# Optimization experiments

Hardware: AMD Instinct MI355X
Metric: run time of the kernel (lower is better)

The kernel has to match this reference:

```python
import jax, jax.numpy as jnp
import numpy as np

N = 50000      # num nodes
E = 800000     # num edges (avg degree 16)
IN_FEA = 256
OU_FEA = 64


def setup_inputs() -> dict:
    key = jax.random.key(0)
    k_h, k_w, k_r, k_c, k_v = jax.random.split(key, 5)
    h = jax.random.normal(k_h, (N, IN_FEA), dtype=jnp.float32)
    # Linear(in_fea, ou_fea, bias=None): weight applied as h @ W, W [IN, OUT]
    W = jax.random.normal(k_w, (IN_FEA, OU_FEA), dtype=jnp.float32) / np.sqrt(IN_FEA)
    row = jax.random.randint(k_r, (E,), 0, N, dtype=jnp.int32)
    col = jax.random.randint(k_c, (E,), 0, N, dtype=jnp.int32)
    vals = jax.random.uniform(k_v, (E,), dtype=jnp.float32)
    return {"h": h, "W": W, "row": row, "col": col, "vals": vals}


def reference(h, W, row, col, vals):
    # dense projection: [N, IN] @ [IN, OUT] -> [N, OUT]
    hp = h @ W
    # torch builds sparse tensor with indices [col, row], i.e. G = A^T,
    # so torch.sparse.mm(G, hp)[i] = sum over edges with col==i of vals * hp[row]
    msg = hp[row] * vals[:, None]                      # [E, OUT] gather + scale
    out = jax.ops.segment_sum(msg, col, num_segments=N)  # scatter-add to dest
    return out
```

## Files before the change

kernel.cpp:

```cpp
#include <hip/hip_runtime.h>
#include <hip/hip_bf16.h>

#define IN_F 256
#define OU_F 64
#define BKN 128
#define BSHIFT 7
#define NBMAX 512
#define CHUNK 4096
#define STAGE_CAP 4096

typedef __attribute__((ext_vector_type(8))) short short8;
typedef __attribute__((ext_vector_type(4))) float f32x4;

__device__ inline short8 cvt8(float4 a, float4 b)
{
    union { short8 s8; __hip_bfloat162 h2[4]; } u;
    u.h2[0] = __float22bfloat162_rn(make_float2(a.x, a.y));
    u.h2[1] = __float22bfloat162_rn(make_float2(a.z, a.w));
    u.h2[2] = __float22bfloat162_rn(make_float2(b.x, b.y));
    u.h2[3] = __float22bfloat162_rn(make_float2(b.z, b.w));
    return u.s8;
}

__global__ void __launch_bounds__(512, 4)
gemm_mfma_kernel(const float* __restrict__ h, const float* __restrict__ W,
                 __hip_bfloat16* __restrict__ hp, int* __restrict__ bcnt,
                 int N, int ntiles)
{
    __shared__ unsigned short Wt[64][264];
    const int t = threadIdx.x;

    if (blockIdx.x == 0)
        for (int i = t; i <= NBMAX; i += 512) bcnt[i] = 0;

#pragma unroll
    for (int i = 0; i < 16; ++i) {
        int p  = t + i * 512;
        int c  = p & 63;
        int k0 = (p >> 6) << 1;
        float x = W[(size_t)k0 * OU_F + c];
        float y = W[(size_t)(k0 + 1) * OU_F + c];
        __hip_bfloat162 bb = __float22bfloat162_rn(make_float2(x, y));
        *reinterpret_cast<unsigned*>(&Wt[c][k0]) = *reinterpret_cast<unsigned*>(&bb);
    }
    __syncthreads();

    const int l   = t & 63;
    const int wv  = t >> 6;
    const int cl  = l & 15;
    const int kg  = l >> 4;
    const int rg4 = wv & 3;
    const int cg  = wv >> 2;

    short8 bfr[2][8];
#pragma unroll
    for (int nt2 = 0; nt2 < 2; ++nt2)
#pragma unroll
        for (int ks = 0; ks < 8; ++ks)
            bfr[nt2][ks] = *reinterpret_cast<const short8*>(
                &Wt[cg * 32 + nt2 * 16 + cl][ks * 32 + kg * 8]);

    for (int tile = blockIdx.x; tile < ntiles; tile += gridDim.x) {
        const int rbase = tile * 64 + rg4 * 16;
        const int r     = rbase + cl;
        const int rld   = min(r, N - 1);
        const float4* hrow = reinterpret_cast<const float4*>(h) + (size_t)rld * (IN_F / 4);

        f32x4 acc0 = (f32x4){0.f, 0.f, 0.f, 0.f};
        f32x4 acc1 = (f32x4){0.f, 0.f, 0.f, 0.f};
#pragma unroll
        for (int ks = 0; ks < 8; ++ks) {
            float4 a0 = hrow[ks * 8 + kg * 2];
            float4 a1 = hrow[ks * 8 + kg * 2 + 1];
            short8 af = cvt8(a0, a1);
            acc0 = __builtin_amdgcn_mfma_f32_16x16x32_bf16(af, bfr[0][ks], acc0, 0, 0, 0);
            acc1 = __builtin_amdgcn_mfma_f32_16x16x32_bf16(af, bfr[1][ks], acc1, 0, 0, 0);
        }

#pragma unroll
        for (int rg = 0; rg < 4; ++rg) {
            int rr = rbase + kg * 4 + rg;
            if (rr < N) {
                size_t base = (size_t)rr * OU_F + cg * 32 + cl;
                hp[base]      = __float2bfloat16(acc0[rg]);
                hp[base + 16] = __float2bfloat16(acc1[rg]);
            }
        }
    }
}

__global__ void __launch_bounds__(256)
hist_scan_kernel(const int* __restrict__ col, int* __restrict__ bcnt,
                 int* __restrict__ boffs, int* __restrict__ bcursor, int E, int NB)
{
    __shared__ int lh[NBMAX];
    __shared__ int s[256];
    __shared__ int isLast;
    const int t = threadIdx.x;

    for (int i = t; i < NB; i += 256) lh[i] = 0;
    __syncthreads();

    const int n4 = E >> 2;
    const int4* c4 = (const int4*)col;
    for (int i = blockIdx.x * 256 + t; i < n4; i += gridDim.x * 256) {
        int4 v = c4[i];
        atomicAdd(&lh[v.x >> BSHIFT], 1);
        atomicAdd(&lh[v.y >> BSHIFT], 1);
        atomicAdd(&lh[v.z >> BSHIFT], 1);
        atomicAdd(&lh[v.w >> BSHIFT], 1);
    }
    if (blockIdx.x == 0)
        for (int e = (n4 << 2) + t; e < E; e += 256)
            atomicAdd(&lh[col[e] >> BSHIFT], 1);
    __syncthreads();

    for (int i = t; i < NB; i += 256)
        if (lh[i]) atomicAdd(&bcnt[i], lh[i]);

    __threadfence();
    if (t == 0) {
        int v = atomicAdd(&bcnt[NBMAX], 1);
        isLast = (v == (int)gridDim.x - 1);
    }
    __syncthreads();
    if (!isLast) return;

    for (int i = t; i < NB; i += 256)
        lh[i] = __hip_atomic_load(&bcnt[i], __ATOMIC_RELAXED, __HIP_MEMORY_SCOPE_AGENT);
    __syncthreads();

    int idx = t * 2;
    int c0 = (idx     < NB) ? lh[idx]     : 0;
    int c1 = (idx + 1 < NB) ? lh[idx + 1] : 0;
    int s0 = c0, s1 = s0 + c1;
    s[t] = s1;
    __syncthreads();
    for (int d = 1; d < 256; d <<= 1) {
        int v = (t >= d) ? s[t - d] : 0;
        __syncthreads();
        s[t] += v;
        __syncthreads();
    }
    int excl = (t > 0) ? s[t - 1] : 0;
    if (idx     < NB) { boffs[idx]     = excl;      bcursor[idx]     = excl;      }
    if (idx + 1 < NB) { boffs[idx + 1] = excl + s0; bcursor[idx + 1] = excl + s0; }
    if (t == 255) boffs[NB] = s[255];
}

__global__ void __launch_bounds__(256)
partition_kernel(const int* __restrict__ row, const int* __restrict__ col,
                 const float* __restrict__ vals, int* __restrict__ bcursor,
                 int2* __restrict__ epk, int E, int NB)
{
    __shared__ int  hist[NBMAX];
    __shared__ int  X[NBMAX];
    __shared__ int  gshift[NBMAX];
    __shared__ int  s[256];
    __shared__ int2 stage[CHUNK];
    __shared__ int  gpos[CHUNK];

    const int t = threadIdx.x;
    const int base = blockIdx.x * CHUNK;
    const int n = min(CHUNK, E - base);

    for (int i = t; i < NBMAX; i += 256) hist[i] = 0;
    __syncthreads();

#pragma unroll
    for (int k = 0; k < CHUNK / 256; ++k) {
        int i = t + k * 256;
        if (i < n) atomicAdd(&hist[col[base + i] >> BSHIFT], 1);
    }
    __syncthreads();

    int idx = t * 2;
    int c0 = hist[idx], c1 = hist[idx + 1];
    int s0 = c0, s1 = s0 + c1;
    s[t] = s1;
    __syncthreads();
    for (int d = 1; d < 256; d <<= 1) {
        int v = (t >= d) ? s[t - d] : 0;
        __syncthreads();
        s[t] += v;
        __syncthreads();
    }
    int excl = (t > 0) ? s[t - 1] : 0;
    X[idx]     = excl;
    X[idx + 1] = excl + s0;
    __syncthreads();

    for (int i = t; i < NB; i += 256) {
        int hcnt = hist[i];
        int g = hcnt ? atomicAdd(&bcursor[i], hcnt) : 0;
        gshift[i] = g - X[i];
    }
    __syncthreads();

#pragma unroll
    for (int k = 0; k < CHUNK / 256; ++k) {
        int i = t + k * 256;
        if (i < n) {
            int e  = base + i;
            int cv = col[e];
            int b  = cv >> BSHIFT;
            int r  = atomicAdd(&X[b], 1);
            unsigned pk = (unsigned)row[e] | ((unsigned)(cv & (BKN - 1)) << 17);
            stage[r] = make_int2((int)pk, __float_as_int(vals[e]));
            gpos[r]  = gshift[b] + r;
        }
    }
    __syncthreads();

#pragma unroll
    for (int k = 0; k < CHUNK / 256; ++k) {
        int i = t + k * 256;
        if (i < n) epk[gpos[i]] = stage[i];
    }
}

__global__ void __launch_bounds__(256)
csr_kernel(const int2* __restrict__ epk, const int* __restrict__ boffs,
           int2* __restrict__ epk2, int* __restrict__ node_offs,
           int N, int NB)
{
    __shared__ int  cnt[BKN];
    __shared__ int  sc[BKN];
    __shared__ int  cur[BKN];
    __shared__ int2 stage[STAGE_CAP];
    const int t = threadIdx.x;
    const int b = blockIdx.x;
    const int s = boffs[b], e = boffs[b + 1];
    const int n = e - s;
    const int node0 = b << BSHIFT;

    if (t < BKN) cnt[t] = 0;
    __syncthreads();
    for (int i = t; i < n; i += 256)
        atomicAdd(&cnt[((unsigned)epk[s + i].x) >> 17], 1);
    __syncthreads();

    if (t < BKN) sc[t] = cnt[t];
    __syncthreads();
    for (int d = 1; d < BKN; d <<= 1) {
        int v = 0;
        if (t < BKN && t >= d) v = sc[t - d];
        __syncthreads();
        if (t < BKN) sc[t] += v;
        __syncthreads();
    }
    if (t < BKN) {
        int excl = sc[t] - cnt[t];
        cur[t] = excl;
        int node = node0 + t;
        if (node < N) node_offs[node] = s + excl;
    }
    if (b == NB - 1 && t == 0) node_offs[N] = e;
    __syncthreads();

    if (n <= STAGE_CAP) {
        for (int i = t; i < n; i += 256) {
            int2 r = epk[s + i];
            int pos = atomicAdd(&cur[((unsigned)r.x) >> 17], 1);
            stage[pos] = r;
        }
        __syncthreads();
        for (int i = t; i < n; i += 256)
            epk2[s + i] = stage[i];
    } else {
        for (int i = t; i < n; i += 256) {
            int2 r = epk[s + i];
            int pos = atomicAdd(&cur[((unsigned)r.x) >> 17], 1);
            epk2[s + pos] = r;
        }
    }
}

__global__ void __launch_bounds__(256)
gather_kernel(const __hip_bfloat16* __restrict__ hp, const int* __restrict__ node_offs,
              const int2* __restrict__ epk2, float* __restrict__ out, int N)
{
    int wid  = (int)((blockIdx.x * 256u + threadIdx.x) >> 6);
    int lane = threadIdx.x & 63;
    if (wid >= N) return;
    int s = node_offs[wid], e = node_offs[wid + 1];
    float acc = 0.f;
    for (int base = s; base < e; base += 64) {
        int n = min(64, e - base);
        int2 m = make_int2(0, 0);
        if (lane < n) m = epk2[base + lane];
        int j = 0;
        for (; j + 4 <= n; j += 4) {
            unsigned r0 = (unsigned)__shfl(m.x, j)     & 0x1FFFFu;
            unsigned r1 = (unsigned)__shfl(m.x, j + 1) & 0x1FFFFu;
            unsigned r2 = (unsigned)__shfl(m.x, j + 2) & 0x1FFFFu;
            unsigned r3 = (unsigned)__shfl(m.x, j + 3) & 0x1FFFFu;
            float v0 = __int_as_float(__shfl(m.y, j));
            float v1 = __int_as_float(__shfl(m.y, j + 1));
            float v2 = __int_as_float(__shfl(m.y, j + 2));
            float v3 = __int_as_float(__shfl(m.y, j + 3));
            float x0 = __bfloat162float(hp[((size_t)r0 << 6) + lane]);
            float x1 = __bfloat162float(hp[((size_t)r1 << 6) + lane]);
            float x2 = __bfloat162float(hp[((size_t)r2 << 6) + lane]);
            float x3 = __bfloat162float(hp[((size_t)r3 << 6) + lane]);
            acc = fmaf(v0, x0, acc);
            acc = fmaf(v1, x1, acc);
            acc = fmaf(v2, x2, acc);
            acc = fmaf(v3, x3, acc);
        }
        for (; j < n; ++j) {
            unsigned r = (unsigned)__shfl(m.x, j) & 0x1FFFFu;
            float    v = __int_as_float(__shfl(m.y, j));
            acc = fmaf(v, __bfloat162float(hp[((size_t)r << 6) + lane]), acc);
        }
    }
    out[(size_t)wid * OU_F + lane] = acc;
}

__global__ void __launch_bounds__(256)
scatter_kernel(const __hip_bfloat16* __restrict__ hp, const int* __restrict__ row,
               const int* __restrict__ col, const float* __restrict__ vals,
               float* __restrict__ out, int E)
{
    unsigned int gid = blockIdx.x * 256u + threadIdx.x;
    int e = (int)(gid >> 6);
    if (e >= E) return;
    int f = (int)(gid & 63u);
    int r = row[e], c = col[e];
    float m = vals[e] * __bfloat162float(hp[(size_t)r * OU_F + f]);
    __hip_atomic_fetch_add(&out[(size_t)c * OU_F + f], m,
                           __ATOMIC_RELAXED, __HIP_MEMORY_SCOPE_AGENT);
}

extern "C" void kernel_launch(void* const* d_in, const int* in_sizes, int n_in,
                              void* d_out, int out_size, void* d_ws, size_t ws_size,
                              hipStream_t stream)
{
    const float* h    = (const float*)d_in[0];
    const float* W    = (const float*)d_in[1];
    const int*   row  = (const int*)d_in[2];
    const int*   col  = (const int*)d_in[3];
    const float* vals = (const float*)d_in[4];
    float*       out  = (float*)d_out;

    const int N = in_sizes[0] / IN_F;
    const int E = in_sizes[2];
    const int NB = (N + BKN - 1) / BKN;

    char*  ws  = (char*)d_ws;
    size_t off = 0;
    auto alloc = [&](size_t bytes) -> char* {
        char* p = ws + off;
        off = (off + bytes + 255) & ~(size_t)255;
        return p;
    };
    __hip_bfloat16* hp = (__hip_bfloat16*)alloc((size_t)N * OU_F * 2);
    int*   bcnt      = (int*)  alloc((size_t)(NBMAX + 1) * 4);
    int*   boffs     = (int*)  alloc((size_t)(NBMAX + 1) * 4);
    int*   bcursor   = (int*)  alloc((size_t)NBMAX * 4);
    int*   node_offs = (int*)  alloc((size_t)(N + 1) * 4);
    int2*  epk       = (int2*) alloc((size_t)E * 8);
    int2*  epk2      = (int2*) alloc((size_t)E * 8);
    const bool fits = (off <= ws_size) && (NB <= NBMAX) && (N < 131072);

    const int ntiles = (N + 63) / 64;
    gemm_mfma_kernel<<<512, 512, 0, stream>>>(h, W, hp, bcnt, N, ntiles);

    if (fits) {
        hist_scan_kernel<<<256, 256, 0, stream>>>(col, bcnt, boffs, bcursor, E, NB);
        partition_kernel<<<(E + CHUNK - 1) / CHUNK, 256, 0, stream>>>(
            row, col, vals, bcursor, epk, E, NB);
        csr_kernel<<<NB, 256, 0, stream>>>(epk, boffs, epk2, node_offs, N, NB);
        gather_kernel<<<(N + 3) / 4, 256, 0, stream>>>(hp, node_offs, epk2, out, N);
    } else {
        hipMemsetAsync(d_out, 0, (size_t)out_size * sizeof(float), stream);
        unsigned long long total = (unsigned long long)E * 64ull;
        unsigned int sgrid = (unsigned int)((total + 255ull) / 256ull);
        scatter_kernel<<<sgrid, 256, 0, stream>>>(hp, row, col, vals, out, E);
    }
}
```

Before: 94.50 us.

## Launch one GEMM tile per block, widen partition/CSR blocks, shuffle-based CSR scan

The GEMM now launches one block per 64-row tile instead of a 512-block grid-stride loop. Each block reloads and converts W, so that setup is now repeated for roughly 782 tiles. The partition and CSR kernels move from 256 to 512 threads per block, so each thread handles fewer elements. The CSR kernel's multi-barrier shared-memory scan becomes a single-wavefront shuffle scan. The aim is more parallelism and fewer barriers in the preprocessing kernels, at the cost of redundant W loads in the GEMM.

```diff
diff --git a/kernel.cpp b/kernel.cpp
--- a/kernel.cpp
+++ b/kernel.cpp
@@ -24,8 +24,7 @@
 
 __global__ void __launch_bounds__(512, 4)
 gemm_mfma_kernel(const float* __restrict__ h, const float* __restrict__ W,
-                 __hip_bfloat16* __restrict__ hp, int* __restrict__ bcnt,
-                 int N, int ntiles)
+                 __hip_bfloat16* __restrict__ hp, int* __restrict__ bcnt, int N)
 {
     __shared__ unsigned short Wt[64][264];
     const int t = threadIdx.x;
@@ -60,31 +59,29 @@
             bfr[nt2][ks] = *reinterpret_cast<const short8*>(
                 &Wt[cg * 32 + nt2 * 16 + cl][ks * 32 + kg * 8]);
 
-    for (int tile = blockIdx.x; tile < ntiles; tile += gridDim.x) {
-        const int rbase = tile * 64 + rg4 * 16;
-        const int r     = rbase + cl;
-        const int rld   = min(r, N - 1);
-        const float4* hrow = reinterpret_cast<const float4*>(h) + (size_t)rld * (IN_F / 4);
-
-        f32x4 acc0 = (f32x4){0.f, 0.f, 0.f, 0.f};
-        f32x4 acc1 = (f32x4){0.f, 0.f, 0.f, 0.f};
-#pragma unroll
-        for (int ks = 0; ks < 8; ++ks) {
-            float4 a0 = hrow[ks * 8 + kg * 2];
-            float4 a1 = hrow[ks * 8 + kg * 2 + 1];
-            short8 af = cvt8(a0, a1);
-            acc0 = __builtin_amdgcn_mfma_f32_16x16x32_bf16(af, bfr[0][ks], acc0, 0, 0, 0);
-            acc1 = __builtin_amdgcn_mfma_f32_16x16x32_bf16(af, bfr[1][ks], acc1, 0, 0, 0);
-        }
-
-#pragma unroll
-        for (int rg = 0; rg < 4; ++rg) {
-            int rr = rbase + kg * 4 + rg;
-            if (rr < N) {
-                size_t base = (size_t)rr * OU_F + cg * 32 + cl;
-                hp[base]      = __float2bfloat16(acc0[rg]);
-                hp[base + 16] = __float2bfloat16(acc1[rg]);
-            }
+    const int rbase = blockIdx.x * 64 + rg4 * 16;
+    const int r     = rbase + cl;
+    const int rld   = min(r, N - 1);
+    const float4* hrow = reinterpret_cast<const float4*>(h) + (size_t)rld * (IN_F / 4);
+
+    f32x4 acc0 = (f32x4){0.f, 0.f, 0.f, 0.f};
+    f32x4 acc1 = (f32x4){0.f, 0.f, 0.f, 0.f};
+#pragma unroll
+    for (int ks = 0; ks < 8; ++ks) {
+        float4 a0 = hrow[ks * 8 + kg * 2];
+        float4 a1 = hrow[ks * 8 + kg * 2 + 1];
+        short8 af = cvt8(a0, a1);
+        acc0 = __builtin_amdgcn_mfma_f32_16x16x32_bf16(af, bfr[0][ks], acc0, 0, 0, 0);
+        acc1 = __builtin_amdgcn_mfma_f32_16x16x32_bf16(af, bfr[1][ks], acc1, 0, 0, 0);
+    }
+
+#pragma unroll
+    for (int rg = 0; rg < 4; ++rg) {
+        int rr = rbase + kg * 4 + rg;
+        if (rr < N) {
+            size_t base = (size_t)rr * OU_F + cg * 32 + cl;
+            hp[base]      = __float2bfloat16(acc0[rg]);
+            hp[base + 16] = __float2bfloat16(acc1[rg]);
         }
     }
 }
@@ -148,7 +145,7 @@
     if (t == 255) boffs[NB] = s[255];
 }
 
-__global__ void __launch_bounds__(256)
+__global__ void __launch_bounds__(512)
 partition_kernel(const int* __restrict__ row, const int* __restrict__ col,
                  const float* __restrict__ vals, int* __restrict__ bcursor,
                  int2* __restrict__ epk, int E, int NB)
@@ -164,33 +161,38 @@
     const int base = blockIdx.x * CHUNK;
     const int n = min(CHUNK, E - base);
 
-    for (int i = t; i < NBMAX; i += 256) hist[i] = 0;
-    __syncthreads();
-
-#pragma unroll
-    for (int k = 0; k < CHUNK / 256; ++k) {
-        int i = t + k * 256;
+    for (int i = t; i < NBMAX; i += 512) hist[i] = 0;
+    __syncthreads();
+
+#pragma unroll
+    for (int k = 0; k < CHUNK / 512; ++k) {
+        int i = t + k * 512;
         if (i < n) atomicAdd(&hist[col[base + i] >> BSHIFT], 1);
     }
     __syncthreads();
 
-    int idx = t * 2;
-    int c0 = hist[idx], c1 = hist[idx + 1];
-    int s0 = c0, s1 = s0 + c1;
-    s[t] = s1;
+    int s0 = 0, s1 = 0;
+    if (t < 256) {
+        int idx = t * 2;
+        s0 = hist[idx];
+        s1 = s0 + hist[idx + 1];
+        s[t] = s1;
+    }
     __syncthreads();
     for (int d = 1; d < 256; d <<= 1) {
-        int v = (t >= d) ? s[t - d] : 0;
-        __syncthreads();
-        s[t] += v;
-        __syncthreads();
-    }
-    int excl = (t > 0) ? s[t - 1] : 0;
-    X[idx]     = excl;
-    X[idx + 1] = excl + s0;
-    __syncthreads();
-
-    for (int i = t; i < NB; i += 256) {
+        int v = (t >= d && t < 256) ? s[t - d] : 0;
+        __syncthreads();
+        if (t < 256) s[t] += v;
+        __syncthreads();
+    }
+    if (t < 256) {
+        int excl = (t > 0) ? s[t - 1] : 0;
+        X[t * 2]     = excl;
+        X[t * 2 + 1] = excl + s0;
+    }
+    __syncthreads();
+
+    for (int i = t; i < NB; i += 512) {
         int hcnt = hist[i];
         int g = hcnt ? atomicAdd(&bcursor[i], hcnt) : 0;
         gshift[i] = g - X[i];
@@ -198,8 +200,8 @@
     __syncthreads();
 
 #pragma unroll
-    for (int k = 0; k < CHUNK / 256; ++k) {
-        int i = t + k * 256;
+    for (int k = 0; k < CHUNK / 512; ++k) {
+        int i = t + k * 512;
         if (i < n) {
             int e  = base + i;
             int cv = col[e];
@@ -213,19 +215,18 @@
     __syncthreads();
 
 #pragma unroll
-    for (int k = 0; k < CHUNK / 256; ++k) {
-        int i = t + k * 256;
+    for (int k = 0; k < CHUNK / 512; ++k) {
+        int i = t + k * 512;
         if (i < n) epk[gpos[i]] = stage[i];
     }
 }
 
-__global__ void __launch_bounds__(256)
+__global__ void __launch_bounds__(512)
 csr_kernel(const int2* __restrict__ epk, const int* __restrict__ boffs,
            int2* __restrict__ epk2, int* __restrict__ node_offs,
            int N, int NB)
 {
     __shared__ int  cnt[BKN];
-    __shared__ int  sc[BKN];
     __shared__ int  cur[BKN];
     __shared__ int2 stage[STAGE_CAP];
     const int t = threadIdx.x;
@@ -236,39 +237,39 @@
 
     if (t < BKN) cnt[t] = 0;
     __syncthreads();
-    for (int i = t; i < n; i += 256)
+    for (int i = t; i < n; i += 512)
         atomicAdd(&cnt[((unsigned)epk[s + i].x) >> 17], 1);
     __syncthreads();
 
-    if (t < BKN) sc[t] = cnt[t];
-    __syncthreads();
-    for (int d = 1; d < BKN; d <<= 1) {
-        int v = 0;
-        if (t < BKN && t >= d) v = sc[t - d];
-        __syncthreads();
-        if (t < BKN) sc[t] += v;
-        __syncthreads();
-    }
-    if (t < BKN) {
-        int excl = sc[t] - cnt[t];
-        cur[t] = excl;
-        int node = node0 + t;
-        if (node < N) node_offs[node] = s + excl;
+    if (t < 64) {
+        int v0 = cnt[2 * t], v1 = cnt[2 * t + 1];
+        int p = v0 + v1, sum = p;
+#pragma unroll
+        for (int d = 1; d < 64; d <<= 1) {
+            int u = __shfl_up(sum, d);
+            if (t >= d) sum += u;
+        }
+        int excl = sum - p;
+        cur[2 * t]     = excl;
+        cur[2 * t + 1] = excl + v0;
+        int nd0 = node0 + 2 * t;
+        if (nd0 < N)     node_offs[nd0]     = s + excl;
+        if (nd0 + 1 < N) node_offs[nd0 + 1] = s + excl + v0;
     }
     if (b == NB - 1 && t == 0) node_offs[N] = e;
     __syncthreads();
 
     if (n <= STAGE_CAP) {
-        for (int i = t; i < n; i += 256) {
+        for (int i = t; i < n; i += 512) {
             int2 r = epk[s + i];
             int pos = atomicAdd(&cur[((unsigned)r.x) >> 17], 1);
             stage[pos] = r;
         }
         __syncthreads();
-        for (int i = t; i < n; i += 256)
+        for (int i = t; i < n; i += 512)
             epk2[s + i] = stage[i];
     } else {
-        for (int i = t; i < n; i += 256) {
+        for (int i = t; i < n; i += 512) {
             int2 r = epk[s + i];
             int pos = atomicAdd(&cur[((unsigned)r.x) >> 17], 1);
             epk2[s + pos] = r;
@@ -364,13 +365,13 @@
     const bool fits = (off <= ws_size) && (NB <= NBMAX) && (N < 131072);
 
     const int ntiles = (N + 63) / 64;
-    gemm_mfma_kernel<<<512, 512, 0, stream>>>(h, W, hp, bcnt, N, ntiles);
+    gemm_mfma_kernel<<<ntiles, 512, 0, stream>>>(h, W, hp, bcnt, N);
 
     if (fits) {
         hist_scan_kernel<<<256, 256, 0, stream>>>(col, bcnt, boffs, bcursor, E, NB);
-        partition_kernel<<<(E + CHUNK - 1) / CHUNK, 256, 0, stream>>>(
+        partition_kernel<<<(E + CHUNK - 1) / CHUNK, 512, 0, stream>>>(
             row, col, vals, bcursor, epk, E, NB);
-        csr_kernel<<<NB, 256, 0, stream>>>(epk, boffs, epk2, node_offs, N, NB);
+        csr_kernel<<<NB, 512, 0, stream>>>(epk, boffs, epk2, node_offs, N, NB);
         gather_kernel<<<(N + 3) / 4, 256, 0, stream>>>(hp, node_offs, epk2, out, N);
     } else {
         hipMemsetAsync(d_out, 0, (size_t)out_size * sizeof(float), stream);
```

New measurement: 90.00 us. -4.8%, faster.
